# Kernel tuning notes

Hardware: AMD Instinct MI355X
Metric: run time of the kernel (lower is better)

## Reference

```python
import jax, jax.numpy as jnp
import numpy as np

D = 2048      # d_model
QH = 32       # query heads
KVH = 8       # kv heads
HD = D // QH  # head_dim = 64
B = 2
S = 2048
THETA = 1000000.0


def _rope_cos_sin(seq_len, hd, dtype):
    inv_freq = 1.0 / (THETA ** (jnp.arange(0, hd, 2, dtype=jnp.float32) / hd))
    t = jnp.arange(seq_len, dtype=jnp.float32)
    freqs = jnp.einsum('i,j->ij', t, inv_freq)          # [S, hd/2]
    emb = jnp.concatenate([freqs, freqs], axis=-1)      # [S, hd]
    cos = jnp.cos(emb)[None, :, None, :].astype(dtype)  # [1,S,1,hd]
    sin = jnp.sin(emb)[None, :, None, :].astype(dtype)
    return cos, sin


def _rotate_half(x):
    half = x.shape[-1] // 2
    x1, x2 = x[..., :half], x[..., half:]
    return jnp.concatenate([-x2, x1], axis=-1)


def setup_inputs() -> dict:
    key = jax.random.key(0)
    ks = jax.random.split(key, 9)
    inp = {
        'q': jax.random.normal(ks[0], (B, S, D), dtype=jnp.float32),
        'k': jax.random.normal(ks[1], (B, S, D), dtype=jnp.float32),
        'v': jax.random.normal(ks[2], (B, S, D), dtype=jnp.float32),
        'attn_mask': jnp.ones((B, S), dtype=jnp.float32),  # ignored by source math
        'Wq': jax.random.normal(ks[3], (D, D), dtype=jnp.float32) * 0.02,
        'Wk': jax.random.normal(ks[4], (D, KVH * HD), dtype=jnp.float32) * 0.02,
        'Wv': jax.random.normal(ks[5], (D, KVH * HD), dtype=jnp.float32) * 0.02,
        'Wo': jax.random.normal(ks[6], (D, D), dtype=jnp.float32) * 0.02,
        'bo': jnp.zeros((D,), dtype=jnp.float32),
    }
    return inp


def reference(q, k, v, attn_mask, Wq, Wk, Wv, Wo, bo):
    b, s, _ = q.shape
    qh = (q @ Wq).reshape(b, s, QH, HD)
    kh = (k @ Wk).reshape(b, s, KVH, HD)
    vh = (v @ Wv).reshape(b, s, KVH, HD)

    cos, sin = _rope_cos_sin(s, HD, qh.dtype)
    qh = qh * cos + _rotate_half(qh) * sin
    kh = kh * cos + _rotate_half(kh) * sin

    g = QH // KVH
    # torch .repeat tiles the head axis: [h0..h7, h0..h7, ...]
    kh = jnp.tile(kh, (1, 1, g, 1))  # [b,s,QH,HD]
    vh = jnp.tile(vh, (1, 1, g, 1))

    qt = qh.transpose(0, 2, 1, 3)  # [b,QH,s,HD]
    kt = kh.transpose(0, 2, 1, 3)
    vt = vh.transpose(0, 2, 1, 3)

    scale = 1.0 / jnp.sqrt(jnp.asarray(HD, dtype=qt.dtype))
    scores = jnp.einsum('bhqd,bhkd->bhqk', qt, kt) * scale
    # source passes attn_mask=None, is_causal=False when a mask is given:
    # full non-causal attention, mask value unused.
    attn = jax.nn.softmax(scores, axis=-1)
    out = jnp.einsum('bhqk,bhkd->bhqd', attn, vt)
    out = out.transpose(0, 2, 1, 3).reshape(b, s, D)
    return out @ Wo + bo
```

## Files before the change

### kernel.cpp

```cpp
#include <hip/hip_runtime.h>
#include <math.h>

#define D_    2048
#define QH_   32
#define KVH_  8
#define HD_   64
#define B_    2
#define S_    2048
#define NROW_ (B_*S_)
#define KVD_  (KVH_*HD_)
#define LOG2E 1.44269504f

typedef __bf16 bf16;
typedef __bf16 bf16x2 __attribute__((ext_vector_type(2)));
typedef __bf16 bf16x4 __attribute__((ext_vector_type(4)));
typedef __bf16 bf16x8 __attribute__((ext_vector_type(8)));
typedef float  f32x4  __attribute__((ext_vector_type(4)));
typedef float  f32x16 __attribute__((ext_vector_type(16)));

__device__ __forceinline__ f32x4 mfma16(bf16x8 a, bf16x8 b, f32x4 c) {
  return __builtin_amdgcn_mfma_f32_16x16x32_bf16(a, b, c, 0, 0, 0);
}
__device__ __forceinline__ f32x16 mfma32(bf16x8 a, bf16x8 b, f32x16 c) {
  return __builtin_amdgcn_mfma_f32_32x32x16_bf16(a, b, c, 0, 0, 0);
}

__device__ __forceinline__ void gload_lds16(const bf16* g, bf16* l) {
  __builtin_amdgcn_global_load_lds(
      (const __attribute__((address_space(1))) void*)g,
      (__attribute__((address_space(3))) void*)l, 16, 0, 0);
}

__device__ __forceinline__ unsigned pack_bf16(float a, float b) {
  union { bf16x2 v; unsigned u; } t;
  t.v[0] = (bf16)a; t.v[1] = (bf16)b;
  return t.u;
}

__global__ void k_ropetab(float2* __restrict__ tab) {
  int idx = blockIdx.x * 256 + threadIdx.x;
  int s = idx >> 5, d = idx & 31;
  float invf = exp2f(-(float)d * 0.62286151f);
  float ang = (float)s * invf;
  float sn, cs;
  sincosf(ang, &sn, &cs);
  tab[idx] = make_float2(cs, sn);
}

__device__ __forceinline__ void transpose_w_body(const float* W, bf16* Wt, int K, int N) {
  __shared__ float tile[32][33];
  int n0 = blockIdx.x * 32, k0 = blockIdx.y * 32;
  int tx = threadIdx.x, ty = threadIdx.y;
#pragma unroll
  for (int j = 0; j < 4; j++)
    tile[ty + 8*j][tx] = W[(size_t)(k0 + ty + 8*j) * N + n0 + tx];
  __syncthreads();
#pragma unroll
  for (int j = 0; j < 4; j++)
    Wt[(size_t)(n0 + ty + 8*j) * K + k0 + tx] = (bf16)tile[tx][ty + 8*j];
}

__global__ void k_transpose_w(const float* __restrict__ W, bf16* __restrict__ Wt,
                              int K, int N) {
  transpose_w_body(W, Wt, K, N);
}

__global__ void k_transpose_w2(const float* __restrict__ W0, const float* __restrict__ W1,
                               bf16* __restrict__ T0, bf16* __restrict__ T1) {
  transpose_w_body(blockIdx.z ? W1 : W0, blockIdx.z ? T1 : T0, D_, KVD_);
}

template<int EPI>
__device__ __forceinline__ void gemm_body(bf16* Asb, bf16* Bsb,
                                          const bf16* A, const bf16* Bt, void* Cout,
                                          const float* bias, const float2* tab,
                                          int M, int N, int K) {
  int tid = threadIdx.x;
  int wave = tid >> 6, lane = tid & 63, hi = lane >> 4, lr = lane & 15;
  int wm = wave >> 1, wn = wave & 1;
  int m0 = blockIdx.y * 128, n0 = blockIdx.x * 128;
  f32x4 acc[4][4] = {};
  int nk = K >> 6;

  int s_row[4], s_dch[4];
#pragma unroll
  for (int i = 0; i < 4; i++) {
    int c = i * 256 + tid;
    s_row[i] = c >> 3;
    s_dch[i] = (c & 7) ^ (s_row[i] & 7);
  }

#define GSTAGE(buf, kt_)                                                       \
  do {                                                                         \
    int k0_ = (kt_) * 64;                                                      \
    _Pragma("unroll")                                                          \
    for (int i = 0; i < 4; i++) {                                              \
      gload_lds16(A  + (size_t)(m0 + s_row[i]) * K + k0_ + s_dch[i] * 8,       \
                  Asb + ((buf) * 8192 + (i * 256 + wave * 64) * 8));           \
      gload_lds16(Bt + (size_t)(n0 + s_row[i]) * K + k0_ + s_dch[i] * 8,       \
                  Bsb + ((buf) * 8192 + (i * 256 + wave * 64) * 8));           \
    }                                                                          \
  } while (0)

  GSTAGE(0, 0);
  __syncthreads();

  for (int kt = 0; kt < nk; kt++) {
    int cur = kt & 1;
    if (kt + 1 < nk) GSTAGE(cur ^ 1, kt + 1);
#pragma unroll
    for (int kk = 0; kk < 2; kk++) {
      bf16x8 af[4], bfr[4];
#pragma unroll
      for (int mt = 0; mt < 4; mt++) {
        int row = wm * 64 + mt * 16 + lr;
        int sl = (kk * 4 + hi) ^ (row & 7);
        af[mt] = *(const bf16x8*)(Asb + cur * 8192 + row * 64 + sl * 8);
      }
#pragma unroll
      for (int nt = 0; nt < 4; nt++) {
        int row = wn * 64 + nt * 16 + lr;
        int sl = (kk * 4 + hi) ^ (row & 7);
        bfr[nt] = *(const bf16x8*)(Bsb + cur * 8192 + row * 64 + sl * 8);
      }
      __builtin_amdgcn_s_setprio(1);
#pragma unroll
      for (int mt = 0; mt < 4; mt++)
#pragma unroll
        for (int nt = 0; nt < 4; nt++)
          acc[mt][nt] = mfma16(af[mt], bfr[nt], acc[mt][nt]);
      __builtin_amdgcn_s_setprio(0);
    }
    __syncthreads();
  }
#undef GSTAGE

#pragma unroll
  for (int mt = 0; mt < 4; mt++)
#pragma unroll
    for (int nt = 0; nt < 4; nt++)
#pragma unroll
      for (int r = 0; r < 4; r++) {
        int grow = m0 + wm * 64 + mt * 16 + 4 * hi + r;
        int gcol = n0 + wn * 64 + nt * 16 + lr;
        ((float*)Cout)[(size_t)grow * N + gcol] = acc[mt][nt][r] + bias[gcol];
      }
}

__global__ __launch_bounds__(256) void k_gemm_q(const float* __restrict__ Af,
                                                const bf16* __restrict__ Bt,
                                                bf16* __restrict__ C,
                                                const float2* __restrict__ tab) {
  __shared__ alignas(16) bf16 As[2][128 * 64];
  __shared__ alignas(16) bf16 Bs[2][128 * 64];
  bf16* Asb = &As[0][0];
  bf16* Bsb = &Bs[0][0];
  const int M = NROW_, N = D_, K = D_;
  int tid = threadIdx.x;
  int wave = tid >> 6, lane = tid & 63, hi = lane >> 4, lr = lane & 15;
  int wm = wave >> 1, wn = wave & 1;
  int m0 = blockIdx.y * 128, n0 = blockIdx.x * 128;
  f32x4 acc[4][4] = {};
  const int nk = K >> 6;

  int s_row[4], s_dch[4];
#pragma unroll
  for (int i = 0; i < 4; i++) {
    int c = i * 256 + tid;
    s_row[i] = c >> 3;
    s_dch[i] = (c & 7) ^ (s_row[i] & 7);
  }

  f32x4 areg[4][2];

#define A_LOADQ(kt_)                                                           \
  do {                                                                         \
    int k0_ = (kt_) * 64;                                                      \
    _Pragma("unroll")                                                          \
    for (int i = 0; i < 4; i++) {                                              \
      const float* p = Af + (size_t)(m0 + s_row[i]) * K + k0_ + s_dch[i] * 8;  \
      areg[i][0] = *(const f32x4*)p;                                           \
      areg[i][1] = *(const f32x4*)(p + 4);                                     \
    }                                                                          \
  } while (0)

#define A_WRITEQ(buf)                                                          \
  do {                                                                         \
    _Pragma("unroll")                                                          \
    for (int i = 0; i < 4; i++) {                                              \
      bf16x8 v;                                                                \
      _Pragma("unroll")                                                        \
      for (int j = 0; j < 4; j++) {                                            \
        v[j]     = (bf16)areg[i][0][j];                                        \
        v[4 + j] = (bf16)areg[i][1][j];                                        \
      }                                                                        \
      *(bf16x8*)(Asb + (buf) * 8192 + (i * 256 + tid) * 8) = v;                \
    }                                                                          \
  } while (0)

#define GSTAGE_BQ(buf, kt_)                                                    \
  do {                                                                         \
    int k0_ = (kt_) * 64;                                                      \
    _Pragma("unroll")                                                          \
    for (int i = 0; i < 4; i++)                                                \
      gload_lds16(Bt + (size_t)(n0 + s_row[i]) * K + k0_ + s_dch[i] * 8,       \
                  Bsb + ((buf) * 8192 + (i * 256 + wave * 64) * 8));           \
  } while (0)

  A_LOADQ(0);
  GSTAGE_BQ(0, 0);
  A_WRITEQ(0);
  __syncthreads();

  for (int kt = 0; kt < nk; kt++) {
    int cur = kt & 1;
    if (kt + 1 < nk) {
      A_LOADQ(kt + 1);
      GSTAGE_BQ(cur ^ 1, kt + 1);
    }
#pragma unroll
    for (int kk = 0; kk < 2; kk++) {
      bf16x8 af[4], bfr[4];
#pragma unroll
      for (int mt = 0; mt < 4; mt++) {
        int row = wm * 64 + mt * 16 + lr;
        int sl = (kk * 4 + hi) ^ (row & 7);
        af[mt] = *(const bf16x8*)(Asb + cur * 8192 + row * 64 + sl * 8);
      }
#pragma unroll
      for (int nt = 0; nt < 4; nt++) {
        int row = wn * 64 + nt * 16 + lr;
        int sl = (kk * 4 + hi) ^ (row & 7);
        bfr[nt] = *(const bf16x8*)(Bsb + cur * 8192 + row * 64 + sl * 8);
      }
      __builtin_amdgcn_s_setprio(1);
#pragma unroll
      for (int mt = 0; mt < 4; mt++)
#pragma unroll
        for (int nt = 0; nt < 4; nt++)
          acc[mt][nt] = mfma16(af[mt], bfr[nt], acc[mt][nt]);
      __builtin_amdgcn_s_setprio(0);
    }
    if (kt + 1 < nk) A_WRITEQ(cur ^ 1);
    __syncthreads();
  }
#undef A_LOADQ
#undef A_WRITEQ
#undef GSTAGE_BQ

#pragma unroll
  for (int mt = 0; mt < 4; mt++)
#pragma unroll
    for (int r = 0; r < 4; r++) {
      int grow = m0 + wm * 64 + mt * 16 + 4 * hi + r;
      int s = grow & (S_ - 1);
#pragma unroll
      for (int nt = 0; nt < 2; nt++) {
        int gcol = n0 + wn * 64 + nt * 16 + lr;
        float2 cs = tab[s * 32 + nt * 16 + lr];
        float x1 = acc[mt][nt][r], x2 = acc[mt][nt + 2][r];
        C[(size_t)grow * N + gcol]      = (bf16)(x1 * cs.x - x2 * cs.y);
        C[(size_t)grow * N + gcol + 32] = (bf16)(x2 * cs.x + x1 * cs.y);
      }
    }
}

__global__ __launch_bounds__(256) void k_gemm_o(const bf16* __restrict__ A,
                                                const bf16* __restrict__ Bt,
                                                float* __restrict__ C,
                                                const float* __restrict__ bias) {
  __shared__ alignas(16) bf16 As[2][128 * 64];
  __shared__ alignas(16) bf16 Bs[2][128 * 64];
  gemm_body<2>(&As[0][0], &Bs[0][0], A, Bt, C, bias, nullptr, NROW_, D_, D_);
}

template<int EPI>
__device__ __forceinline__ void gemm_body64(bf16* Asb, bf16* Bsb,
                                            const float* Af, const bf16* Bt, void* Cout,
                                            const float2* tab) {
  const int K = D_, N = KVD_;
  int tid = threadIdx.x;
  int wave = tid >> 6, lane = tid & 63, hi = lane >> 4, lr = lane & 15;
  int m0 = blockIdx.y * 64, n0 = blockIdx.x * 128;
  int nbase = (wave >> 1) * 64 + (wave & 1) * 16;
  f32x4 acc[4][2] = {};
  const int nk = K >> 6;

  int a_row[2], a_dch[2], b_row[4], b_dch[4];
#pragma unroll
  for (int i = 0; i < 2; i++) {
    int c = i * 256 + tid;
    a_row[i] = c >> 3;
    a_dch[i] = (c & 7) ^ (a_row[i] & 7);
  }
#pragma unroll
  for (int i = 0; i < 4; i++) {
    int c = i * 256 + tid;
    b_row[i] = c >> 3;
    b_dch[i] = (c & 7) ^ (b_row[i] & 7);
  }

  f32x4 areg[2][2];

#define A_LOAD(kt_)                                                            \
  do {                                                                         \
    int k0_ = (kt_) * 64;                                                      \
    _Pragma("unroll")                                                          \
    for (int i = 0; i < 2; i++) {                                              \
      const float* p = Af + (size_t)(m0 + a_row[i]) * K + k0_ + a_dch[i] * 8;  \
      areg[i][0] = *(const f32x4*)p;                                           \
      areg[i][1] = *(const f32x4*)(p + 4);                                     \
    }                                                                          \
  } while (0)

#define A_WRITE(buf)                                                           \
  do {                                                                         \
    _Pragma("unroll")                                                          \
    for (int i = 0; i < 2; i++) {                                              \
      bf16x8 v;                                                                \
      _Pragma("unroll")                                                        \
      for (int j = 0; j < 4; j++) {                                            \
        v[j]     = (bf16)areg[i][0][j];                                        \
        v[4 + j] = (bf16)areg[i][1][j];                                        \
      }                                                                        \
      *(bf16x8*)(Asb + (buf) * 4096 + (i * 256 + tid) * 8) = v;                \
    }                                                                          \
  } while (0)

#define GSTAGE_B(buf, kt_)                                                     \
  do {                                                                         \
    int k0_ = (kt_) * 64;                                                      \
    _Pragma("unroll")                                                          \
    for (int i = 0; i < 4; i++)                                                \
      gload_lds16(Bt + (size_t)(n0 + b_row[i]) * K + k0_ + b_dch[i] * 8,       \
                  Bsb + ((buf) * 8192 + (i * 256 + wave * 64) * 8));           \
  } while (0)

  A_LOAD(0);
  GSTAGE_B(0, 0);
  A_WRITE(0);
  __syncthreads();

  for (int kt = 0; kt < nk; kt++) {
    int cur = kt & 1;
    if (kt + 1 < nk) {
      A_LOAD(kt + 1);
      GSTAGE_B(cur ^ 1, kt + 1);
    }
#pragma unroll
    for (int kk = 0; kk < 2; kk++) {
      bf16x8 af[4], bfr[2];
#pragma unroll
      for (int mt = 0; mt < 4; mt++) {
        int row = mt * 16 + lr;
        int sl = (kk * 4 + hi) ^ (row & 7);
        af[mt] = *(const bf16x8*)(Asb + cur * 4096 + row * 64 + sl * 8);
      }
#pragma unroll
      for (int nt = 0; nt < 2; nt++) {
        int row = nbase + nt * 32 + lr;
        int sl = (kk * 4 + hi) ^ (row & 7);
        bfr[nt] = *(const bf16x8*)(Bsb + cur * 8192 + row * 64 + sl * 8);
      }
      __builtin_amdgcn_s_setprio(1);
#pragma unroll
      for (int mt = 0; mt < 4; mt++)
#pragma unroll
        for (int nt = 0; nt < 2; nt++) {
          if (EPI == 3) acc[mt][nt] = mfma16(bfr[nt], af[mt], acc[mt][nt]);
          else          acc[mt][nt] = mfma16(af[mt], bfr[nt], acc[mt][nt]);
        }
      __builtin_amdgcn_s_setprio(0);
    }
    if (kt + 1 < nk) A_WRITE(cur ^ 1);
    __syncthreads();
  }
#undef A_LOAD
#undef A_WRITE
#undef GSTAGE_B

  if (EPI == 1) {
#pragma unroll
    for (int mt = 0; mt < 4; mt++)
#pragma unroll
      for (int r = 0; r < 4; r++) {
        int grow = m0 + mt * 16 + 4 * hi + r;
        int s = grow & (S_ - 1);
        int d = (wave & 1) * 16 + lr;
        int gcol = n0 + nbase + lr;
        float2 cs = tab[s * 32 + d];
        float x1 = acc[mt][0][r], x2 = acc[mt][1][r];
        ((bf16*)Cout)[(size_t)grow * N + gcol]      = (bf16)(x1 * cs.x - x2 * cs.y);
        ((bf16*)Cout)[(size_t)grow * N + gcol + 32] = (bf16)(x2 * cs.x + x1 * cs.y);
      }
  } else {
    int b = m0 >> 11;
#pragma unroll
    for (int mt = 0; mt < 4; mt++)
#pragma unroll
      for (int nt = 0; nt < 2; nt++)
#pragma unroll
        for (int r = 0; r < 4; r++) {
          int n = n0 + nbase + nt * 32 + 4 * hi + r;
          int m = m0 + mt * 16 + lr;
          ((bf16*)Cout)[((size_t)(b * KVD_ + n)) * S_ + (m & (S_ - 1))] =
              (bf16)acc[mt][nt][r];
        }
  }
}

__global__ __launch_bounds__(256) void k_gemm_kv(const float* __restrict__ kf,
                                                 const float* __restrict__ vf,
                                                 const bf16* __restrict__ B0,
                                                 const bf16* __restrict__ B1,
                                                 bf16* __restrict__ Kh,
                                                 bf16* __restrict__ Vt,
                                                 const float2* __restrict__ tab) {
  __shared__ alignas(16) bf16 As[2][64 * 64];
  __shared__ alignas(16) bf16 Bs[2][128 * 64];
  if (blockIdx.z == 0) gemm_body64<1>(&As[0][0], &Bs[0][0], kf, B0, Kh, tab);
  else                 gemm_body64<3>(&As[0][0], &Bs[0][0], vf, B1, Vt, nullptr);
}

__global__ __launch_bounds__(512, 4) void k_attn(const bf16* __restrict__ Qh,
                                                 const bf16* __restrict__ Kh,
                                                 const bf16* __restrict__ Vt,
                                                 bf16* __restrict__ ctx) {
  __shared__ alignas(16) bf16 Ks[2][64 * 64];
  __shared__ alignas(16) bf16 Vs[2][64 * 64];
  int tid = threadIdx.x;
  int wave = tid >> 6, lane = tid & 63, hi2 = lane >> 5, l31 = lane & 31;
  int qt = blockIdx.x, h = blockIdx.y, b = blockIdx.z;
  int kv = h & 7;
  int q0 = qt * 256 + wave * 32;

  bf16x8 qf[4];
  {
    const float QSC = 0.125f * LOG2E;
    const bf16* qp = Qh + (size_t)(b * S_ + q0 + l31) * D_ + h * HD_ + hi2 * 8;
#pragma unroll
    for (int df = 0; df < 4; df++) {
      bf16x8 v = *(const bf16x8*)(qp + 16 * df);
#pragma unroll
      for (int j = 0; j < 8; j++) v[j] = (bf16)((float)v[j] * QSC);
      qf[df] = v;
    }
  }

  float l_run = 0.f;
  f32x16 o0, o1;
#pragma unroll
  for (int i = 0; i < 16; i++) { o0[i] = 0.f; o1[i] = 0.f; }

  const bf16* Kg = Kh + (size_t)(b * S_) * KVD_ + kv * HD_;
  const bf16* Vg = Vt + (size_t)(b * KVH_ + kv) * HD_ * S_;

  int c_row = tid >> 3, c_slot = tid & 7;
  int c_dch = c_slot ^ (c_row & 7);

#define STAGE(buf, kt_)                                                        \
  do {                                                                         \
    gload_lds16(Kg + (size_t)((kt_) * 64 + c_row) * KVD_ + c_dch * 8,          \
                &Ks[buf][tid * 8]);                                            \
    gload_lds16(Vg + (size_t)c_row * S_ + (kt_) * 64 + c_dch * 8,              \
                &Vs[buf][tid * 8]);                                            \
  } while (0)

  STAGE(0, 0);
  __syncthreads();

  const int NT = S_ / 64;
  for (int kt = 0; kt < NT; kt++) {
    int cur = kt & 1;
    if (kt + 1 < NT) STAGE(cur ^ 1, kt + 1);

    const bf16* Kb = &Ks[cur][0];
    const bf16* Vb = &Vs[cur][0];

    f32x16 s0, s1;
#pragma unroll
    for (int i = 0; i < 16; i++) { s0[i] = 0.f; s1[i] = 0.f; }
    __builtin_amdgcn_s_setprio(1);
#pragma unroll
    for (int df = 0; df < 4; df++) {
      int ch = hi2 + 2 * df;
      int sl = (ch ^ (l31 & 7)) << 3;
      bf16x8 k0 = *(const bf16x8*)(Kb + l31 * 64 + sl);
      bf16x8 k1 = *(const bf16x8*)(Kb + (l31 + 32) * 64 + sl);
      s0 = mfma32(k0, qf[df], s0);
      s1 = mfma32(k1, qf[df], s1);
    }
    __builtin_amdgcn_s_setprio(0);

    float rs = 0.f;
#pragma unroll
    for (int i = 0; i < 16; i++) { s0[i] = __builtin_amdgcn_exp2f(s0[i]); rs += s0[i]; }
#pragma unroll
    for (int i = 0; i < 16; i++) { s1[i] = __builtin_amdgcn_exp2f(s1[i]); rs += s1[i]; }
    l_run += rs;

    unsigned Rk[2][4][2];
#pragma unroll
    for (int m = 0; m < 4; m++)
#pragma unroll
      for (int w = 0; w < 2; w++) {
        Rk[0][m][w] = pack_bf16(s0[4*m + 2*w], s0[4*m + 2*w + 1]);
        Rk[1][m][w] = pack_bf16(s1[4*m + 2*w], s1[4*m + 2*w + 1]);
      }
#pragma unroll
    for (int kf = 0; kf < 2; kf++)
#pragma unroll
      for (int kp = 0; kp < 2; kp++)
#pragma unroll
        for (int w = 0; w < 2; w++)
          asm volatile("v_permlane32_swap_b32 %0, %1"
                       : "+v"(Rk[kf][2*kp][w]), "+v"(Rk[kf][2*kp+1][w]));
    bf16x8 pf[4];
#pragma unroll
    for (int kfr = 0; kfr < 4; kfr++) {
      int kf = kfr >> 1, k2 = (kfr & 1) * 2;
      union { unsigned d[4]; bf16x8 v; } u;
      u.d[0] = Rk[kf][k2][0];     u.d[1] = Rk[kf][k2][1];
      u.d[2] = Rk[kf][k2 + 1][0]; u.d[3] = Rk[kf][k2 + 1][1];
      pf[kfr] = u.v;
    }

    __builtin_amdgcn_s_setprio(1);
#pragma unroll
    for (int kfr = 0; kfr < 4; kfr++) {
      int ch = hi2 + 2 * kfr;
      int sl = (ch ^ (l31 & 7)) << 3;
      bf16x8 v0 = *(const bf16x8*)(Vb + l31 * 64 + sl);
      bf16x8 v1 = *(const bf16x8*)(Vb + (l31 + 32) * 64 + sl);
      o0 = mfma32(pf[kfr], v0, o0);
      o1 = mfma32(pf[kfr], v1, o1);
    }
    __builtin_amdgcn_s_setprio(0);
    __syncthreads();
  }
#undef STAGE

  float l_full = l_run + __shfl_xor(l_run, 32, 64);
#pragma unroll
  for (int r = 0; r < 16; r++) {
    int rowq = (r & 3) + 8 * (r >> 2) + 4 * hi2;
    float inv = 1.f / __shfl(l_full, rowq, 64);
    size_t base = (size_t)(b * S_ + q0 + rowq) * D_ + h * HD_;
    ctx[base + l31]      = (bf16)(o0[r] * inv);
    ctx[base + l31 + 32] = (bf16)(o1[r] * inv);
  }
}

extern "C" void kernel_launch(void* const* d_in, const int* in_sizes, int n_in,
                              void* d_out, int out_size, void* d_ws, size_t ws_size,
                              hipStream_t stream) {
  const float* q  = (const float*)d_in[0];
  const float* k  = (const float*)d_in[1];
  const float* v  = (const float*)d_in[2];
  const float* Wq = (const float*)d_in[4];
  const float* Wk = (const float*)d_in[5];
  const float* Wv = (const float*)d_in[6];
  const float* Wo = (const float*)d_in[7];
  const float* bo = (const float*)d_in[8];

  char* ws = (char*)d_ws;
  bf16*   A1  = (bf16*)(ws + 16777216);
  bf16*   Wt  = (bf16*)(ws + 33554432);
  bf16*   Qh  = (bf16*)(ws + 41943040);
  bf16*   Kh  = (bf16*)(ws + 58720256);
  bf16*   Vt  = (bf16*)(ws + 62914560);
  float2* tab = (float2*)(ws + 67108864);
  bf16*   WtK = Wt;
  bf16*   WtV = (bf16*)(ws + 33554432 + 2097152);
  bf16*   ctx = A1;

  k_ropetab<<<(S_ * 32) / 256, 256, 0, stream>>>(tab);
  k_transpose_w<<<dim3(D_/32, D_/32), dim3(32, 8), 0, stream>>>(Wq, Wt, D_, D_);
  k_gemm_q<<<dim3(D_/128, NROW_/128), 256, 0, stream>>>(q, Wt, Qh, tab);
  k_transpose_w2<<<dim3(KVD_/32, D_/32, 2), dim3(32, 8), 0, stream>>>(Wk, Wv, WtK, WtV);
  k_gemm_kv<<<dim3(KVD_/128, NROW_/64, 2), 256, 0, stream>>>(k, v, WtK, WtV, Kh, Vt, tab);
  k_attn<<<dim3(S_/256, QH_, B_), 512, 0, stream>>>(Qh, Kh, Vt, ctx);
  k_transpose_w<<<dim3(D_/32, D_/32), dim3(32, 8), 0, stream>>>(Wo, Wt, D_, D_);
  k_gemm_o<<<dim3(D_/128, NROW_/128), 256, 0, stream>>>(ctx, Wt, (float*)d_out, bo);
}
```

Baseline: 240.7 us.

## Merge weight prep and QKV projections into fewer launches; row-sum via MFMA

Folds the rope table build and all four weight transposes into one prep launch, and runs the Q, K and V projection GEMMs together in a single grid split on blockIdx.z, dropping the launch count from eight to four. The goal is less launch overhead and fewer idle tails, with the small K/V GEMMs sharing the machine with the Q GEMM. In attention, the softmax row sum now comes from an extra MFMA against a vector of ones rather than scalar adds and cross-lane shuffles. The fused grid launches many blocks that exit immediately, and the extra MFMA per tile adds matrix-unit work in exchange for fewer VALU ops.

```diff
diff --git a/kernel.cpp b/kernel.cpp
--- a/kernel.cpp
+++ b/kernel.cpp
@@ -13,7 +13,6 @@
 
 typedef __bf16 bf16;
 typedef __bf16 bf16x2 __attribute__((ext_vector_type(2)));
-typedef __bf16 bf16x4 __attribute__((ext_vector_type(4)));
 typedef __bf16 bf16x8 __attribute__((ext_vector_type(8)));
 typedef float  f32x4  __attribute__((ext_vector_type(4)));
 typedef float  f32x16 __attribute__((ext_vector_type(16)));
@@ -37,16 +36,6 @@
   return t.u;
 }
 
-__global__ void k_ropetab(float2* __restrict__ tab) {
-  int idx = blockIdx.x * 256 + threadIdx.x;
-  int s = idx >> 5, d = idx & 31;
-  float invf = exp2f(-(float)d * 0.62286151f);
-  float ang = (float)s * invf;
-  float sn, cs;
-  sincosf(ang, &sn, &cs);
-  tab[idx] = make_float2(cs, sn);
-}
-
 __device__ __forceinline__ void transpose_w_body(const float* W, bf16* Wt, int K, int N) {
   __shared__ float tile[32][33];
   int n0 = blockIdx.x * 32, k0 = blockIdx.y * 32;
@@ -60,102 +49,36 @@
     Wt[(size_t)(n0 + ty + 8*j) * K + k0 + tx] = (bf16)tile[tx][ty + 8*j];
 }
 
-__global__ void k_transpose_w(const float* __restrict__ W, bf16* __restrict__ Wt,
-                              int K, int N) {
-  transpose_w_body(W, Wt, K, N);
-}
-
-__global__ void k_transpose_w2(const float* __restrict__ W0, const float* __restrict__ W1,
-                               bf16* __restrict__ T0, bf16* __restrict__ T1) {
-  transpose_w_body(blockIdx.z ? W1 : W0, blockIdx.z ? T1 : T0, D_, KVD_);
-}
-
-template<int EPI>
-__device__ __forceinline__ void gemm_body(bf16* Asb, bf16* Bsb,
-                                          const bf16* A, const bf16* Bt, void* Cout,
-                                          const float* bias, const float2* tab,
-                                          int M, int N, int K) {
-  int tid = threadIdx.x;
-  int wave = tid >> 6, lane = tid & 63, hi = lane >> 4, lr = lane & 15;
-  int wm = wave >> 1, wn = wave & 1;
-  int m0 = blockIdx.y * 128, n0 = blockIdx.x * 128;
-  f32x4 acc[4][4] = {};
-  int nk = K >> 6;
-
-  int s_row[4], s_dch[4];
-#pragma unroll
-  for (int i = 0; i < 4; i++) {
-    int c = i * 256 + tid;
-    s_row[i] = c >> 3;
-    s_dch[i] = (c & 7) ^ (s_row[i] & 7);
-  }
-
-#define GSTAGE(buf, kt_)                                                       \
-  do {                                                                         \
-    int k0_ = (kt_) * 64;                                                      \
-    _Pragma("unroll")                                                          \
-    for (int i = 0; i < 4; i++) {                                              \
-      gload_lds16(A  + (size_t)(m0 + s_row[i]) * K + k0_ + s_dch[i] * 8,       \
-                  Asb + ((buf) * 8192 + (i * 256 + wave * 64) * 8));           \
-      gload_lds16(Bt + (size_t)(n0 + s_row[i]) * K + k0_ + s_dch[i] * 8,       \
-                  Bsb + ((buf) * 8192 + (i * 256 + wave * 64) * 8));           \
-    }                                                                          \
-  } while (0)
-
-  GSTAGE(0, 0);
-  __syncthreads();
-
-  for (int kt = 0; kt < nk; kt++) {
-    int cur = kt & 1;
-    if (kt + 1 < nk) GSTAGE(cur ^ 1, kt + 1);
-#pragma unroll
-    for (int kk = 0; kk < 2; kk++) {
-      bf16x8 af[4], bfr[4];
-#pragma unroll
-      for (int mt = 0; mt < 4; mt++) {
-        int row = wm * 64 + mt * 16 + lr;
-        int sl = (kk * 4 + hi) ^ (row & 7);
-        af[mt] = *(const bf16x8*)(Asb + cur * 8192 + row * 64 + sl * 8);
-      }
-#pragma unroll
-      for (int nt = 0; nt < 4; nt++) {
-        int row = wn * 64 + nt * 16 + lr;
-        int sl = (kk * 4 + hi) ^ (row & 7);
-        bfr[nt] = *(const bf16x8*)(Bsb + cur * 8192 + row * 64 + sl * 8);
-      }
-      __builtin_amdgcn_s_setprio(1);
-#pragma unroll
-      for (int mt = 0; mt < 4; mt++)
-#pragma unroll
-        for (int nt = 0; nt < 4; nt++)
-          acc[mt][nt] = mfma16(af[mt], bfr[nt], acc[mt][nt]);
-      __builtin_amdgcn_s_setprio(0);
-    }
-    __syncthreads();
-  }
-#undef GSTAGE
-
-#pragma unroll
-  for (int mt = 0; mt < 4; mt++)
-#pragma unroll
-    for (int nt = 0; nt < 4; nt++)
-#pragma unroll
-      for (int r = 0; r < 4; r++) {
-        int grow = m0 + wm * 64 + mt * 16 + 4 * hi + r;
-        int gcol = n0 + wn * 64 + nt * 16 + lr;
-        ((float*)Cout)[(size_t)grow * N + gcol] = acc[mt][nt][r] + bias[gcol];
-      }
-}
-
-__global__ __launch_bounds__(256) void k_gemm_q(const float* __restrict__ Af,
-                                                const bf16* __restrict__ Bt,
-                                                bf16* __restrict__ C,
-                                                const float2* __restrict__ tab) {
-  __shared__ alignas(16) bf16 As[2][128 * 64];
-  __shared__ alignas(16) bf16 Bs[2][128 * 64];
-  bf16* Asb = &As[0][0];
-  bf16* Bsb = &Bs[0][0];
-  const int M = NROW_, N = D_, K = D_;
+__global__ void k_prep(const float* __restrict__ Wq, const float* __restrict__ Wk,
+                       const float* __restrict__ Wv, const float* __restrict__ Wo,
+                       bf16* __restrict__ WtQ, bf16* __restrict__ WtK,
+                       bf16* __restrict__ WtV, bf16* __restrict__ WtO,
+                       float2* __restrict__ tab) {
+  int z = blockIdx.z, x = blockIdx.x, y = blockIdx.y;
+  if (z == 0) {
+    transpose_w_body(Wq, WtQ, D_, D_);
+  } else if (z == 1) {
+    if (x < 16) transpose_w_body(Wk, WtK, D_, KVD_);
+    else if (x < 32 && y < 16) {
+      int r = (x - 16) * 16 + y;
+      int idx = r * 256 + threadIdx.y * 32 + threadIdx.x;
+      int s = idx >> 5, d = idx & 31;
+      float invf = exp2f(-(float)d * 0.62286151f);
+      float sn, cs;
+      sincosf((float)s * invf, &sn, &cs);
+      tab[idx] = make_float2(cs, sn);
+    }
+  } else if (z == 2) {
+    if (x < 16) transpose_w_body(Wv, WtV, D_, KVD_);
+  } else {
+    transpose_w_body(Wo, WtO, D_, D_);
+  }
+}
+
+__device__ __forceinline__ void qproj_body(bf16* Asb, bf16* Bsb,
+                                           const float* Af, const bf16* Bt,
+                                           bf16* C, const float2* tab) {
+  const int N = D_, K = D_;
   int tid = threadIdx.x;
   int wave = tid >> 6, lane = tid & 63, hi = lane >> 4, lr = lane & 15;
   int wm = wave >> 1, wn = wave & 1;
@@ -263,15 +186,6 @@
         C[(size_t)grow * N + gcol + 32] = (bf16)(x2 * cs.x + x1 * cs.y);
       }
     }
-}
-
-__global__ __launch_bounds__(256) void k_gemm_o(const bf16* __restrict__ A,
-                                                const bf16* __restrict__ Bt,
-                                                float* __restrict__ C,
-                                                const float* __restrict__ bias) {
-  __shared__ alignas(16) bf16 As[2][128 * 64];
-  __shared__ alignas(16) bf16 Bs[2][128 * 64];
-  gemm_body<2>(&As[0][0], &Bs[0][0], A, Bt, C, bias, nullptr, NROW_, D_, D_);
 }
 
 template<int EPI>
@@ -409,17 +323,110 @@
   }
 }
 
-__global__ __launch_bounds__(256) void k_gemm_kv(const float* __restrict__ kf,
-                                                 const float* __restrict__ vf,
-                                                 const bf16* __restrict__ B0,
-                                                 const bf16* __restrict__ B1,
-                                                 bf16* __restrict__ Kh,
-                                                 bf16* __restrict__ Vt,
-                                                 const float2* __restrict__ tab) {
-  __shared__ alignas(16) bf16 As[2][64 * 64];
+__global__ __launch_bounds__(256) void k_gemm_qkv(const float* __restrict__ q,
+                                                  const float* __restrict__ k,
+                                                  const float* __restrict__ v,
+                                                  const bf16* __restrict__ WtQ,
+                                                  const bf16* __restrict__ WtK,
+                                                  const bf16* __restrict__ WtV,
+                                                  bf16* __restrict__ Qh,
+                                                  bf16* __restrict__ Kh,
+                                                  bf16* __restrict__ Vt,
+                                                  const float2* __restrict__ tab) {
+  __shared__ alignas(16) bf16 As[2][128 * 64];
   __shared__ alignas(16) bf16 Bs[2][128 * 64];
-  if (blockIdx.z == 0) gemm_body64<1>(&As[0][0], &Bs[0][0], kf, B0, Kh, tab);
-  else                 gemm_body64<3>(&As[0][0], &Bs[0][0], vf, B1, Vt, nullptr);
+  int z = blockIdx.z;
+  if (z == 0) {
+    if (blockIdx.y >= 32) return;
+    qproj_body(&As[0][0], &Bs[0][0], q, WtQ, Qh, tab);
+  } else if (z == 1) {
+    if (blockIdx.x >= 4) return;
+    gemm_body64<1>(&As[0][0], &Bs[0][0], k, WtK, Kh, tab);
+  } else {
+    if (blockIdx.x >= 4) return;
+    gemm_body64<3>(&As[0][0], &Bs[0][0], v, WtV, Vt, nullptr);
+  }
+}
+
+__global__ __launch_bounds__(256) void k_gemm_o(const bf16* __restrict__ A,
+                                                const bf16* __restrict__ Bt,
+                                                float* __restrict__ C,
+                                                const float* __restrict__ bias) {
+  __shared__ alignas(16) bf16 As[2][128 * 64];
+  __shared__ alignas(16) bf16 Bs[2][128 * 64];
+  bf16* Asb = &As[0][0];
+  bf16* Bsb = &Bs[0][0];
+  const int N = D_, K = D_;
+  int tid = threadIdx.x;
+  int wave = tid >> 6, lane = tid & 63, hi = lane >> 4, lr = lane & 15;
+  int wm = wave >> 1, wn = wave & 1;
+  int m0 = blockIdx.y * 128, n0 = blockIdx.x * 128;
+  f32x4 acc[4][4] = {};
+  const int nk = K >> 6;
+
+  int s_row[4], s_dch[4];
+#pragma unroll
+  for (int i = 0; i < 4; i++) {
+    int c = i * 256 + tid;
+    s_row[i] = c >> 3;
+    s_dch[i] = (c & 7) ^ (s_row[i] & 7);
+  }
+
+#define GSTAGE(buf, kt_)                                                       \
+  do {                                                                         \
+    int k0_ = (kt_) * 64;                                                      \
+    _Pragma("unroll")                                                          \
+    for (int i = 0; i < 4; i++) {                                              \
+      gload_lds16(A  + (size_t)(m0 + s_row[i]) * K + k0_ + s_dch[i] * 8,       \
+                  Asb + ((buf) * 8192 + (i * 256 + wave * 64) * 8));           \
+      gload_lds16(Bt + (size_t)(n0 + s_row[i]) * K + k0_ + s_dch[i] * 8,       \
+                  Bsb + ((buf) * 8192 + (i * 256 + wave * 64) * 8));           \
+    }                                                                          \
+  } while (0)
+
+  GSTAGE(0, 0);
+  __syncthreads();
+
+  for (int kt = 0; kt < nk; kt++) {
+    int cur = kt & 1;
+    if (kt + 1 < nk) GSTAGE(cur ^ 1, kt + 1);
+#pragma unroll
+    for (int kk = 0; kk < 2; kk++) {
+      bf16x8 af[4], bfr[4];
+#pragma unroll
+      for (int mt = 0; mt < 4; mt++) {
+        int row = wm * 64 + mt * 16 + lr;
+        int sl = (kk * 4 + hi) ^ (row & 7);
+        af[mt] = *(const bf16x8*)(Asb + cur * 8192 + row * 64 + sl * 8);
+      }
+#pragma unroll
+      for (int nt = 0; nt < 4; nt++) {
+        int row = wn * 64 + nt * 16 + lr;
+        int sl = (kk * 4 + hi) ^ (row & 7);
+        bfr[nt] = *(const bf16x8*)(Bsb + cur * 8192 + row * 64 + sl * 8);
+      }
+      __builtin_amdgcn_s_setprio(1);
+#pragma unroll
+      for (int mt = 0; mt < 4; mt++)
+#pragma unroll
+        for (int nt = 0; nt < 4; nt++)
+          acc[mt][nt] = mfma16(af[mt], bfr[nt], acc[mt][nt]);
+      __builtin_amdgcn_s_setprio(0);
+    }
+    __syncthreads();
+  }
+#undef GSTAGE
+
+#pragma unroll
+  for (int mt = 0; mt < 4; mt++)
+#pragma unroll
+    for (int nt = 0; nt < 4; nt++)
+#pragma unroll
+      for (int r = 0; r < 4; r++) {
+        int grow = m0 + wm * 64 + mt * 16 + 4 * hi + r;
+        int gcol = n0 + wn * 64 + nt * 16 + lr;
+        C[(size_t)grow * N + gcol] = acc[mt][nt][r] + bias[gcol];
+      }
 }
 
 __global__ __launch_bounds__(512, 4) void k_attn(const bf16* __restrict__ Qh,
@@ -447,10 +454,12 @@
     }
   }
 
-  float l_run = 0.f;
-  f32x16 o0, o1;
-#pragma unroll
-  for (int i = 0; i < 16; i++) { o0[i] = 0.f; o1[i] = 0.f; }
+  f32x16 o0, o1, accl;
+#pragma unroll
+  for (int i = 0; i < 16; i++) { o0[i] = 0.f; o1[i] = 0.f; accl[i] = 0.f; }
+  bf16x8 ones;
+#pragma unroll
+  for (int j = 0; j < 8; j++) ones[j] = (bf16)1.0f;
 
   const bf16* Kg = Kh + (size_t)(b * S_) * KVD_ + kv * HD_;
   const bf16* Vg = Vt + (size_t)(b * KVH_ + kv) * HD_ * S_;
@@ -492,12 +501,10 @@
     }
     __builtin_amdgcn_s_setprio(0);
 
-    float rs = 0.f;
-#pragma unroll
-    for (int i = 0; i < 16; i++) { s0[i] = __builtin_amdgcn_exp2f(s0[i]); rs += s0[i]; }
-#pragma unroll
-    for (int i = 0; i < 16; i++) { s1[i] = __builtin_amdgcn_exp2f(s1[i]); rs += s1[i]; }
-    l_run += rs;
+#pragma unroll
+    for (int i = 0; i < 16; i++) s0[i] = __builtin_amdgcn_exp2f(s0[i]);
+#pragma unroll
+    for (int i = 0; i < 16; i++) s1[i] = __builtin_amdgcn_exp2f(s1[i]);
 
     unsigned Rk[2][4][2];
 #pragma unroll
@@ -534,17 +541,17 @@
       bf16x8 v1 = *(const bf16x8*)(Vb + (l31 + 32) * 64 + sl);
       o0 = mfma32(pf[kfr], v0, o0);
       o1 = mfma32(pf[kfr], v1, o1);
+      accl = mfma32(pf[kfr], ones, accl);
     }
     __builtin_amdgcn_s_setprio(0);
     __syncthreads();
   }
 #undef STAGE
 
-  float l_full = l_run + __shfl_xor(l_run, 32, 64);
 #pragma unroll
   for (int r = 0; r < 16; r++) {
     int rowq = (r & 3) + 8 * (r >> 2) + 4 * hi2;
-    float inv = 1.f / __shfl(l_full, rowq, 64);
+    float inv = 1.f / accl[r];
     size_t base = (size_t)(b * S_ + q0 + rowq) * D_ + h * HD_;
     ctx[base + l31]      = (bf16)(o0[r] * inv);
     ctx[base + l31 + 32] = (bf16)(o1[r] * inv);
@@ -564,22 +571,20 @@
   const float* bo = (const float*)d_in[8];
 
   char* ws = (char*)d_ws;
-  bf16*   A1  = (bf16*)(ws + 16777216);
-  bf16*   Wt  = (bf16*)(ws + 33554432);
+  bf16*   WtO = (bf16*)(ws + 0);
+  bf16*   WtK = (bf16*)(ws + 8388608);
+  bf16*   WtV = (bf16*)(ws + 10485760);
+  bf16*   ctx = (bf16*)(ws + 16777216);
+  bf16*   WtQ = (bf16*)(ws + 33554432);
   bf16*   Qh  = (bf16*)(ws + 41943040);
   bf16*   Kh  = (bf16*)(ws + 58720256);
   bf16*   Vt  = (bf16*)(ws + 62914560);
   float2* tab = (float2*)(ws + 67108864);
-  bf16*   WtK = Wt;
-  bf16*   WtV = (bf16*)(ws + 33554432 + 2097152);
-  bf16*   ctx = A1;
-
-  k_ropetab<<<(S_ * 32) / 256, 256, 0, stream>>>(tab);
-  k_transpose_w<<<dim3(D_/32, D_/32), dim3(32, 8), 0, stream>>>(Wq, Wt, D_, D_);
-  k_gemm_q<<<dim3(D_/128, NROW_/128), 256, 0, stream>>>(q, Wt, Qh, tab);
-  k_transpose_w2<<<dim3(KVD_/32, D_/32, 2), dim3(32, 8), 0, stream>>>(Wk, Wv, WtK, WtV);
-  k_gemm_kv<<<dim3(KVD_/128, NROW_/64, 2), 256, 0, stream>>>(k, v, WtK, WtV, Kh, Vt, tab);
+
+  k_prep<<<dim3(64, 64, 4), dim3(32, 8), 0, stream>>>(Wq, Wk, Wv, Wo,
+                                                      WtQ, WtK, WtV, WtO, tab);
+  k_gemm_qkv<<<dim3(16, 64, 3), 256, 0, stream>>>(q, k, v, WtQ, WtK, WtV,
+                                                  Qh, Kh, Vt, tab);
   k_attn<<<dim3(S_/256, QH_, B_), 512, 0, stream>>>(Qh, Kh, Vt, ctx);
-  k_transpose_w<<<dim3(D_/32, D_/32), dim3(32, 8), 0, stream>>>(Wo, Wt, D_, D_);
-  k_gemm_o<<<dim3(D_/128, NROW_/128), 256, 0, stream>>>(ctx, Wt, (float*)d_out, bo);
-}
+  k_gemm_o<<<dim3(D_/128, NROW_/128), 256, 0, stream>>>(ctx, WtO, (float*)d_out, bo);
+}
```

Result: slower. 319.3 us (+32.6%).
